# Optimization experiments

Hardware: AMD Instinct MI355X
Metric: run time of the kernel (lower is better)

Reference implementation:

```python
import jax, jax.numpy as jnp
import numpy as np

B = 262144
L, NO, NW = 5, 5, 3          # num_layers, num_ops, num_widths
AD = L * NO * NW             # arch_dim = 75
D, H = 64, 4                 # embed_dim, num_heads
HD = D // H                  # head_dim = 16
EPS = 1e-5


def _ln(x, g, b):
    m = x.mean(-1, keepdims=True)
    v = ((x - m) ** 2).mean(-1, keepdims=True)
    return (x - m) / jnp.sqrt(v + EPS) * g + b


def setup_inputs() -> dict:
    key = jax.random.key(0)
    ks = jax.random.split(key, 16)
    s = 0.05
    return {
        "hw_idx": jax.random.randint(ks[0], (B,), 0, 4),
        "op_indices": jax.random.randint(ks[1], (B, L), 0, NO),
        "width_indices": jax.random.randint(ks[2], (B, L), 0, NW),
        "hw_embed": jax.random.normal(ks[3], (4, D)) * s,
        "W1": jax.random.normal(ks[4], (128, AD)) * s, "b1": jnp.zeros((128,)),
        "W2": jax.random.normal(ks[5], (D, 128)) * s, "b2": jnp.zeros((D,)),
        "ln1_g": jnp.ones((D,)), "ln1_b": jnp.zeros((D,)),
        "in_proj_w": jax.random.normal(ks[6], (3 * D, D)) * s,
        "in_proj_b": jnp.zeros((3 * D,)),
        "out_proj_w": jax.random.normal(ks[7], (D, D)) * s,
        "out_proj_b": jnp.zeros((D,)),
        "ln2_g": jnp.ones((D,)), "ln2_b": jnp.zeros((D,)),
        "W3": jax.random.normal(ks[8], (32, D)) * s, "b3": jnp.zeros((32,)),
        "W4": jax.random.normal(ks[9], (1, 32)) * s, "b4": jnp.zeros((1,)),
    }


def reference(hw_idx, op_indices, width_indices, hw_embed, W1, b1, W2, b2,
              ln1_g, ln1_b, in_proj_w, in_proj_b, out_proj_w, out_proj_b,
              ln2_g, ln2_b, W3, b3, W4, b4):
    # hardware embedding lookup -> [B, D]
    hw_emb = hw_embed[hw_idx]
    # vectorized one-hot arch encoding: [B, L*NO*NW]
    cell = op_indices * NW + width_indices                  # [B, L]
    onehot = jax.nn.one_hot(cell, NO * NW, dtype=jnp.float32).reshape(-1, AD)
    # arch encoder MLP + LayerNorm (dropout = identity at eval)
    h = jax.nn.relu(onehot @ W1.T + b1)
    arch_emb = _ln(h @ W2.T + b2, ln1_g, ln1_b)             # [B, D]
    # combined sequence of 2 tokens: [B, 2, D]
    combined = jnp.stack([hw_emb, arch_emb], axis=1)
    # multi-head self-attention (torch MultiheadAttention, batch_first)
    qkv = combined @ in_proj_w.T + in_proj_b                # [B, 2, 3D]
    q, k, v = jnp.split(qkv, 3, axis=-1)
    q = q.reshape(-1, 2, H, HD); k = k.reshape(-1, 2, H, HD); v = v.reshape(-1, 2, H, HD)
    scores = jnp.einsum('bqhd,bkhd->bhqk', q, k) / np.sqrt(HD)
    attn = jax.nn.softmax(scores, axis=-1)
    ctx = jnp.einsum('bhqk,bkhd->bqhd', attn, v).reshape(-1, 2, D)
    attn_out = ctx @ out_proj_w.T + out_proj_b
    # residual + LayerNorm, mean-pool over the 2 tokens
    x = _ln(attn_out + combined, ln2_g, ln2_b)
    pooled = x.mean(axis=1)                                 # [B, D]
    # prediction head
    latency = jax.nn.relu(pooled @ W3.T + b3) @ W4.T + b4   # [B, 1]
    return latency
```

## Files before the change

### kernel.cpp

```cpp
#include <hip/hip_runtime.h>


using s8v = __attribute__((ext_vector_type(8))) short;
using h8  = __attribute__((ext_vector_type(8))) _Float16;
using f4  = __attribute__((ext_vector_type(4))) float;

#define BTOT 262144

#define WF_W1   0
#define WF_W2   12288
#define WF_IP   20480
#define WF_OP   32768
#define WF_W3   36864
#define WF_HWE  38912

#define OF_ARCH 6400
#define OF_TARG 7552
#define OF_HWI  7680
#define PWS     7696

__device__ __forceinline__ unsigned short f2h(float f) {
  _Float16 h = (_Float16)f;
  return __builtin_bit_cast(unsigned short, h);
}
__device__ __forceinline__ float h2f(unsigned short u) {
  return (float)__builtin_bit_cast(_Float16, u);
}

__device__ __forceinline__ void swz(const float* __restrict__ W,
                                    unsigned short* __restrict__ dst,
                                    int Kreal, int KS, int NT, int t, int stride) {
  const int total = KS * NT * 512;
  for (int i = t; i < total; i += stride) {
    const int j = i & 7, ln = (i >> 3) & 63, fr = i >> 9;
    const int nt = fr % NT, ks = fr / NT;
    const int n = nt * 16 + (ln & 15);
    const int k = ks * 32 + (ln >> 4) * 8 + j;
    dst[i] = (k < Kreal) ? f2h(W[n * Kreal + k]) : (unsigned short)0;
  }
}

__global__ void k_pre(const float* __restrict__ hwe,
                      const float* __restrict__ W1, const float* __restrict__ W2,
                      const float* __restrict__ ipw, const float* __restrict__ opw,
                      const float* __restrict__ W3,
                      unsigned short* __restrict__ ws) {
  const int t = blockIdx.x * 256 + threadIdx.x;
  const int stride = gridDim.x * 256;
  swz(W1,  ws + WF_W1, 75, 3, 8, t, stride);
  swz(W2,  ws + WF_W2, 128, 4, 4, t, stride);
  swz(ipw, ws + WF_IP, 64, 2, 12, t, stride);
  swz(opw, ws + WF_OP, 64, 2, 4, t, stride);
  swz(W3,  ws + WF_W3, 64, 2, 2, t, stride);
  for (int i = t; i < 256; i += stride) ws[WF_HWE + i] = f2h(hwe[i]);
}

__global__ __launch_bounds__(128, 3) void k_fused(
    const int* __restrict__ g_hw,
    const int* __restrict__ g_op, const int* __restrict__ g_wd,
    const float* __restrict__ g_hwe,
    const float* __restrict__ g_b1, const float* __restrict__ g_b2,
    const float* __restrict__ g_ln1g, const float* __restrict__ g_ln1b,
    const float* __restrict__ g_ipb, const float* __restrict__ g_opb,
    const float* __restrict__ g_ln2g, const float* __restrict__ g_ln2b,
    const float* __restrict__ g_b3,  const float* __restrict__ g_W4,
    const float* __restrict__ g_b4,
    const unsigned short* __restrict__ wsf,
    float* __restrict__ g_out) {
  __shared__ __align__(16) unsigned short sm[2 * PWS];
  const int tid = threadIdx.x;
  const int wave = tid >> 6, lane = tid & 63;
  const int quad = lane >> 4, l15 = lane & 15;
  unsigned short* pw = sm + wave * PWS;
  const int m0 = (blockIdx.x * 2 + wave) * 16;

  if (lane < 16) {
    const int smp = m0 + lane;
    pw[OF_HWI + lane] = (unsigned short)g_hw[smp];
#pragma unroll
    for (int l = 0; l < 5; ++l) {
      const int c = 15 * l + g_op[smp * 5 + l] * 3 + g_wd[smp * 5 + l];
      pw[OF_TARG + lane * 8 + l] = (unsigned short)c;
    }
    pw[OF_TARG + lane * 8 + 5] = 0xFFFFu;
    pw[OF_TARG + lane * 8 + 6] = 0xFFFFu;
    pw[OF_TARG + lane * 8 + 7] = 0xFFFFu;
  }
  const s8v trow = *(const s8v*)(pw + OF_TARG + l15 * 8);

  h8 aoh[3];
#pragma unroll
  for (int ks = 0; ks < 3; ++ks) {
    s8v a;
#pragma unroll
    for (int j = 0; j < 8; ++j) {
      const int k = ks * 32 + quad * 8 + j;
      bool hit = false;
#pragma unroll
      for (int l = 0; l < 5; ++l)
        hit = hit || (k == (int)(unsigned short)trow[l]);
      a[j] = hit ? (short)0x3C00 : (short)0;
    }
    aoh[ks] = __builtin_bit_cast(h8, a);
  }

#pragma unroll
  for (int nt = 0; nt < 8; ++nt) {
    f4 acc = {0.f, 0.f, 0.f, 0.f};
#pragma unroll
    for (int ks = 0; ks < 3; ++ks) {
      const h8 bf = *(const h8*)(wsf + WF_W1 + ((ks * 8 + nt) * 64 + lane) * 8);
      acc = __builtin_amdgcn_mfma_f32_16x16x32_f16(aoh[ks], bf, acc, 0, 0, 0);
    }
    const int col = nt * 16 + l15;
    const float bias = g_b1[col];
#pragma unroll
    for (int r = 0; r < 4; ++r) {
      float v = acc[r] + bias;
      v = v > 0.f ? v : 0.f;
      pw[(quad * 4 + r) * 136 + col] = f2h(v);
    }
  }

  h8 a2[4];
#pragma unroll
  for (int ks = 0; ks < 4; ++ks)
    a2[ks] = *(const h8*)(pw + l15 * 136 + ks * 32 + quad * 8);
  f4 acc2[4];
#pragma unroll
  for (int nt = 0; nt < 4; ++nt) {
    f4 acc = {0.f, 0.f, 0.f, 0.f};
#pragma unroll
    for (int ks = 0; ks < 4; ++ks) {
      const h8 bf = *(const h8*)(wsf + WF_W2 + ((ks * 4 + nt) * 64 + lane) * 8);
      acc = __builtin_amdgcn_mfma_f32_16x16x32_f16(a2[ks], bf, acc, 0, 0, 0);
    }
    acc2[nt] = acc;
  }
  {
    float val[4][4];
#pragma unroll
    for (int nt = 0; nt < 4; ++nt) {
      const float bias = g_b2[nt * 16 + l15];
#pragma unroll
      for (int r = 0; r < 4; ++r) val[nt][r] = acc2[nt][r] + bias;
    }
#pragma unroll
    for (int r = 0; r < 4; ++r) {
      float s = val[0][r] + val[1][r] + val[2][r] + val[3][r];
      float q = val[0][r] * val[0][r] + val[1][r] * val[1][r] +
                val[2][r] * val[2][r] + val[3][r] * val[3][r];
#pragma unroll
      for (int off = 1; off <= 8; off <<= 1) {
        s += __shfl_xor(s, off);
        q += __shfl_xor(q, off);
      }
      const float mean = s * (1.f / 64.f);
      const float var  = q * (1.f / 64.f) - mean * mean;
      const float rstd = rsqrtf(var + 1e-5f);
#pragma unroll
      for (int nt = 0; nt < 4; ++nt) {
        const int col = nt * 16 + l15;
        const float gg = g_ln1g[col], bb = g_ln1b[col];
        pw[OF_ARCH + (quad * 4 + r) * 72 + col] =
            f2h((val[nt][r] - mean) * rstd * gg + bb);
      }
    }
  }

  const int hwrow = (int)pw[OF_HWI + l15];
  h8 at0[2], at1[2];
#pragma unroll
  for (int ks = 0; ks < 2; ++ks) {
    at0[ks] = *(const h8*)(wsf + WF_HWE + hwrow * 64 + ks * 32 + quad * 8);
    at1[ks] = *(const h8*)(pw + OF_ARCH + l15 * 72 + ks * 32 + quad * 8);
  }
#pragma unroll
  for (int nt = 0; nt < 12; ++nt) {
    const h8 bf0 = *(const h8*)(wsf + WF_IP + ((0 * 12 + nt) * 64 + lane) * 8);
    const h8 bf1 = *(const h8*)(wsf + WF_IP + ((1 * 12 + nt) * 64 + lane) * 8);
    f4 a0 = {0.f, 0.f, 0.f, 0.f}, a1 = {0.f, 0.f, 0.f, 0.f};
    a0 = __builtin_amdgcn_mfma_f32_16x16x32_f16(at0[0], bf0, a0, 0, 0, 0);
    a0 = __builtin_amdgcn_mfma_f32_16x16x32_f16(at0[1], bf1, a0, 0, 0, 0);
    a1 = __builtin_amdgcn_mfma_f32_16x16x32_f16(at1[0], bf0, a1, 0, 0, 0);
    a1 = __builtin_amdgcn_mfma_f32_16x16x32_f16(at1[1], bf1, a1, 0, 0, 0);
    const int col = nt * 16 + l15;
    const float bias = g_ipb[col];
#pragma unroll
    for (int r = 0; r < 4; ++r) {
      pw[(quad * 4 + r) * 200 + col]      = f2h(a0[r] + bias);
      pw[(16 + quad * 4 + r) * 200 + col] = f2h(a1[r] + bias);
    }
  }

  float ctx[2][16];
  {
    float qv[2][16], kv[2][16], vv[2][16];
#pragma unroll
    for (int tt = 0; tt < 2; ++tt) {
      const unsigned short* base = pw + (tt * 16 + l15) * 200;
#pragma unroll
      for (int c = 0; c < 2; ++c) {
        const h8 qq = *(const h8*)(base + quad * 16 + c * 8);
        const h8 kk = *(const h8*)(base + 64 + quad * 16 + c * 8);
        const h8 vvv = *(const h8*)(base + 128 + quad * 16 + c * 8);
#pragma unroll
        for (int d = 0; d < 8; ++d) {
          qv[tt][c * 8 + d] = (float)qq[d];
          kv[tt][c * 8 + d] = (float)kk[d];
          vv[tt][c * 8 + d] = (float)vvv[d];
        }
      }
    }
    float s00 = 0.f, s01 = 0.f, s10 = 0.f, s11 = 0.f;
#pragma unroll
    for (int d = 0; d < 16; ++d) {
      s00 += qv[0][d] * kv[0][d];
      s01 += qv[0][d] * kv[1][d];
      s10 += qv[1][d] * kv[0][d];
      s11 += qv[1][d] * kv[1][d];
    }
    s00 *= 0.25f; s01 *= 0.25f; s10 *= 0.25f; s11 *= 0.25f;
    const float mA = fmaxf(s00, s01);
    const float e0 = __expf(s00 - mA), e1 = __expf(s01 - mA);
    const float iA = 1.f / (e0 + e1);
    const float a00 = e0 * iA, a01 = e1 * iA;
    const float mB = fmaxf(s10, s11);
    const float f0 = __expf(s10 - mB), f1 = __expf(s11 - mB);
    const float iB = 1.f / (f0 + f1);
    const float a10 = f0 * iB, a11 = f1 * iB;
#pragma unroll
    for (int d = 0; d < 16; ++d) {
      ctx[0][d] = a00 * vv[0][d] + a01 * vv[1][d];
      ctx[1][d] = a10 * vv[0][d] + a11 * vv[1][d];
    }
  }
#pragma unroll
  for (int tt = 0; tt < 2; ++tt)
#pragma unroll
    for (int d = 0; d < 16; d += 2) {
      const unsigned pk = (unsigned)f2h(ctx[tt][d]) |
                          ((unsigned)f2h(ctx[tt][d + 1]) << 16);
      *(unsigned*)(pw + (tt * 16 + l15) * 72 + quad * 16 + d) = pk;
    }

  h8 ca[2][2];
#pragma unroll
  for (int mt = 0; mt < 2; ++mt)
#pragma unroll
    for (int ks = 0; ks < 2; ++ks)
      ca[mt][ks] = *(const h8*)(pw + (mt * 16 + l15) * 72 + ks * 32 + quad * 8);
  f4 oacc[2][4];
#pragma unroll
  for (int nt = 0; nt < 4; ++nt) {
    const h8 bf0 = *(const h8*)(wsf + WF_OP + ((0 * 4 + nt) * 64 + lane) * 8);
    const h8 bf1 = *(const h8*)(wsf + WF_OP + ((1 * 4 + nt) * 64 + lane) * 8);
#pragma unroll
    for (int mt = 0; mt < 2; ++mt) {
      f4 acc = {0.f, 0.f, 0.f, 0.f};
      acc = __builtin_amdgcn_mfma_f32_16x16x32_f16(ca[mt][0], bf0, acc, 0, 0, 0);
      acc = __builtin_amdgcn_mfma_f32_16x16x32_f16(ca[mt][1], bf1, acc, 0, 0, 0);
      oacc[mt][nt] = acc;
    }
  }
  float pool[4][4];
#pragma unroll
  for (int mt = 0; mt < 2; ++mt) {
    float val[4][4];
#pragma unroll
    for (int nt = 0; nt < 4; ++nt) {
      const int col = nt * 16 + l15;
      const float bias = g_opb[col];
#pragma unroll
      for (int r = 0; r < 4; ++r) {
        const int row = quad * 4 + r;
        float res;
        if (mt == 0) {
          const int hr = (int)pw[OF_HWI + row];
          res = g_hwe[hr * 64 + col];
        } else {
          res = h2f(pw[OF_ARCH + row * 72 + col]);
        }
        val[nt][r] = oacc[mt][nt][r] + bias + res;
      }
    }
#pragma unroll
    for (int r = 0; r < 4; ++r) {
      float s = val[0][r] + val[1][r] + val[2][r] + val[3][r];
      float q = val[0][r] * val[0][r] + val[1][r] * val[1][r] +
                val[2][r] * val[2][r] + val[3][r] * val[3][r];
#pragma unroll
      for (int off = 1; off <= 8; off <<= 1) {
        s += __shfl_xor(s, off);
        q += __shfl_xor(q, off);
      }
      const float mean = s * (1.f / 64.f);
      const float var  = q * (1.f / 64.f) - mean * mean;
      const float rstd = rsqrtf(var + 1e-5f);
#pragma unroll
      for (int nt = 0; nt < 4; ++nt) {
        const int col = nt * 16 + l15;
        const float gg = g_ln2g[col], bb = g_ln2b[col];
        const float xn = (val[nt][r] - mean) * rstd * gg + bb;
        if (mt == 0) pool[nt][r] = 0.5f * xn;
        else         pool[nt][r] += 0.5f * xn;
      }
    }
  }
#pragma unroll
  for (int nt = 0; nt < 4; ++nt)
#pragma unroll
    for (int r = 0; r < 4; ++r)
      pw[2304 + (quad * 4 + r) * 72 + nt * 16 + l15] = f2h(pool[nt][r]);

  h8 pa[2];
#pragma unroll
  for (int ks = 0; ks < 2; ++ks)
    pa[ks] = *(const h8*)(pw + 2304 + l15 * 72 + ks * 32 + quad * 8);
  float part[4] = {0.f, 0.f, 0.f, 0.f};
#pragma unroll
  for (int nt = 0; nt < 2; ++nt) {
    const h8 bf0 = *(const h8*)(wsf + WF_W3 + ((0 * 2 + nt) * 64 + lane) * 8);
    const h8 bf1 = *(const h8*)(wsf + WF_W3 + ((1 * 2 + nt) * 64 + lane) * 8);
    f4 acc = {0.f, 0.f, 0.f, 0.f};
    acc = __builtin_amdgcn_mfma_f32_16x16x32_f16(pa[0], bf0, acc, 0, 0, 0);
    acc = __builtin_amdgcn_mfma_f32_16x16x32_f16(pa[1], bf1, acc, 0, 0, 0);
    const int col = nt * 16 + l15;
    const float bias = g_b3[col];
    const float w4v  = g_W4[col];
#pragma unroll
    for (int r = 0; r < 4; ++r) {
      float y = acc[r] + bias;
      y = y > 0.f ? y : 0.f;
      part[r] += y * w4v;
    }
  }
#pragma unroll
  for (int off = 1; off <= 8; off <<= 1)
#pragma unroll
    for (int r = 0; r < 4; ++r)
      part[r] += __shfl_xor(part[r], off);
  const float b4v = g_b4[0];
  if (l15 == 0) {
#pragma unroll
    for (int r = 0; r < 4; ++r)
      g_out[m0 + quad * 4 + r] = part[r] + b4v;
  }
}

extern "C" void kernel_launch(void* const* d_in, const int* in_sizes, int n_in,
                              void* d_out, int out_size, void* d_ws, size_t ws_size,
                              hipStream_t stream) {
  (void)in_sizes; (void)n_in; (void)out_size; (void)ws_size;
  unsigned short* ws = (unsigned short*)d_ws;

  k_pre<<<64, 256, 0, stream>>>(
      (const float*)d_in[3], (const float*)d_in[4], (const float*)d_in[6],
      (const float*)d_in[10], (const float*)d_in[12], (const float*)d_in[16],
      ws);

  k_fused<<<8192, 128, 0, stream>>>(
      (const int*)d_in[0],
      (const int*)d_in[1], (const int*)d_in[2],
      (const float*)d_in[3],
      (const float*)d_in[5], (const float*)d_in[7],
      (const float*)d_in[8], (const float*)d_in[9],
      (const float*)d_in[11], (const float*)d_in[13],
      (const float*)d_in[14], (const float*)d_in[15],
      (const float*)d_in[17], (const float*)d_in[18],
      (const float*)d_in[19],
      ws, (float*)d_out);
}
```

Baseline: 183.5 us.

## Fold b1 into W1, shrink LDS, single-wave blocks, fdot2 attention scores

Folds the first-layer bias b1 into an extra K column of the swizzled W1 weights. The one-hot input now sets a constant-one entry at k=75, so the bias add after the MFMA goes away. The kernel switches to 64-thread single-wave blocks, and the per-block LDS footprint shrinks. To do that, Q/K are stored with a 136 stride and V is kept in registers instead of LDS. Attention scores use packed fp16 fdot2, and softmax weights are exchanged through a small LDS region to compute the context in MFMA layout. The LN1 output is kept in registers for the residual. More registers are live, and fp16 accumulation via fdot2 may change precision slightly.

```diff
diff --git a/kernel.cpp b/kernel.cpp
--- a/kernel.cpp
+++ b/kernel.cpp
@@ -3,6 +3,7 @@
 
 using s8v = __attribute__((ext_vector_type(8))) short;
 using h8  = __attribute__((ext_vector_type(8))) _Float16;
+using h2v = __attribute__((ext_vector_type(2))) _Float16;
 using f4  = __attribute__((ext_vector_type(4))) float;
 
 #define BTOT 262144
@@ -14,10 +15,11 @@
 #define WF_W3   36864
 #define WF_HWE  38912
 
-#define OF_ARCH 6400
-#define OF_TARG 7552
-#define OF_HWI  7680
-#define PWS     7696
+#define OF_WATT 4352
+#define OF_ARCH 4864
+#define OF_TARG 6016
+#define OF_HWI  6144
+#define LDS_TOT 6160
 
 __device__ __forceinline__ unsigned short f2h(float f) {
   _Float16 h = (_Float16)f;
@@ -28,6 +30,7 @@
 }
 
 __device__ __forceinline__ void swz(const float* __restrict__ W,
+                                    const float* __restrict__ bias,
                                     unsigned short* __restrict__ dst,
                                     int Kreal, int KS, int NT, int t, int stride) {
   const int total = KS * NT * 512;
@@ -36,30 +39,34 @@
     const int nt = fr % NT, ks = fr / NT;
     const int n = nt * 16 + (ln & 15);
     const int k = ks * 32 + (ln >> 4) * 8 + j;
-    dst[i] = (k < Kreal) ? f2h(W[n * Kreal + k]) : (unsigned short)0;
+    float v = 0.f;
+    if (k < Kreal) v = W[n * Kreal + k];
+    else if (bias && k == Kreal) v = bias[n];
+    dst[i] = f2h(v);
   }
 }
 
 __global__ void k_pre(const float* __restrict__ hwe,
-                      const float* __restrict__ W1, const float* __restrict__ W2,
+                      const float* __restrict__ W1, const float* __restrict__ b1,
+                      const float* __restrict__ W2,
                       const float* __restrict__ ipw, const float* __restrict__ opw,
                       const float* __restrict__ W3,
                       unsigned short* __restrict__ ws) {
   const int t = blockIdx.x * 256 + threadIdx.x;
   const int stride = gridDim.x * 256;
-  swz(W1,  ws + WF_W1, 75, 3, 8, t, stride);
-  swz(W2,  ws + WF_W2, 128, 4, 4, t, stride);
-  swz(ipw, ws + WF_IP, 64, 2, 12, t, stride);
-  swz(opw, ws + WF_OP, 64, 2, 4, t, stride);
-  swz(W3,  ws + WF_W3, 64, 2, 2, t, stride);
+  swz(W1,  b1,      ws + WF_W1, 75, 3, 8, t, stride);
+  swz(W2,  nullptr, ws + WF_W2, 128, 4, 4, t, stride);
+  swz(ipw, nullptr, ws + WF_IP, 64, 2, 12, t, stride);
+  swz(opw, nullptr, ws + WF_OP, 64, 2, 4, t, stride);
+  swz(W3,  nullptr, ws + WF_W3, 64, 2, 2, t, stride);
   for (int i = t; i < 256; i += stride) ws[WF_HWE + i] = f2h(hwe[i]);
 }
 
-__global__ __launch_bounds__(128, 3) void k_fused(
+__global__ __launch_bounds__(64, 3) void k_fused(
     const int* __restrict__ g_hw,
     const int* __restrict__ g_op, const int* __restrict__ g_wd,
     const float* __restrict__ g_hwe,
-    const float* __restrict__ g_b1, const float* __restrict__ g_b2,
+    const float* __restrict__ g_b2,
     const float* __restrict__ g_ln1g, const float* __restrict__ g_ln1b,
     const float* __restrict__ g_ipb, const float* __restrict__ g_opb,
     const float* __restrict__ g_ln2g, const float* __restrict__ g_ln2b,
@@ -67,12 +74,11 @@
     const float* __restrict__ g_b4,
     const unsigned short* __restrict__ wsf,
     float* __restrict__ g_out) {
-  __shared__ __align__(16) unsigned short sm[2 * PWS];
-  const int tid = threadIdx.x;
-  const int wave = tid >> 6, lane = tid & 63;
+  __shared__ __align__(16) unsigned short sm[LDS_TOT];
+  const int lane = threadIdx.x;
   const int quad = lane >> 4, l15 = lane & 15;
-  unsigned short* pw = sm + wave * PWS;
-  const int m0 = (blockIdx.x * 2 + wave) * 16;
+  unsigned short* pw = sm;
+  const int m0 = blockIdx.x * 16;
 
   if (lane < 16) {
     const int smp = m0 + lane;
@@ -95,7 +101,7 @@
 #pragma unroll
     for (int j = 0; j < 8; ++j) {
       const int k = ks * 32 + quad * 8 + j;
-      bool hit = false;
+      bool hit = (k == 75);
 #pragma unroll
       for (int l = 0; l < 5; ++l)
         hit = hit || (k == (int)(unsigned short)trow[l]);
@@ -113,10 +119,9 @@
       acc = __builtin_amdgcn_mfma_f32_16x16x32_f16(aoh[ks], bf, acc, 0, 0, 0);
     }
     const int col = nt * 16 + l15;
-    const float bias = g_b1[col];
-#pragma unroll
-    for (int r = 0; r < 4; ++r) {
-      float v = acc[r] + bias;
+#pragma unroll
+    for (int r = 0; r < 4; ++r) {
+      float v = acc[r];
       v = v > 0.f ? v : 0.f;
       pw[(quad * 4 + r) * 136 + col] = f2h(v);
     }
@@ -137,6 +142,7 @@
     }
     acc2[nt] = acc;
   }
+  float archres[4][4];
   {
     float val[4][4];
 #pragma unroll
@@ -162,8 +168,9 @@
       for (int nt = 0; nt < 4; ++nt) {
         const int col = nt * 16 + l15;
         const float gg = g_ln1g[col], bb = g_ln1b[col];
-        pw[OF_ARCH + (quad * 4 + r) * 72 + col] =
-            f2h((val[nt][r] - mean) * rstd * gg + bb);
+        const float xn = (val[nt][r] - mean) * rstd * gg + bb;
+        archres[nt][r] = xn;
+        pw[OF_ARCH + (quad * 4 + r) * 72 + col] = f2h(xn);
       }
     }
   }
@@ -175,6 +182,7 @@
     at0[ks] = *(const h8*)(wsf + WF_HWE + hwrow * 64 + ks * 32 + quad * 8);
     at1[ks] = *(const h8*)(pw + OF_ARCH + l15 * 72 + ks * 32 + quad * 8);
   }
+  float vreg[2][4][4];
 #pragma unroll
   for (int nt = 0; nt < 12; ++nt) {
     const h8 bf0 = *(const h8*)(wsf + WF_IP + ((0 * 12 + nt) * 64 + lane) * 8);
@@ -186,62 +194,70 @@
     a1 = __builtin_amdgcn_mfma_f32_16x16x32_f16(at1[1], bf1, a1, 0, 0, 0);
     const int col = nt * 16 + l15;
     const float bias = g_ipb[col];
-#pragma unroll
-    for (int r = 0; r < 4; ++r) {
-      pw[(quad * 4 + r) * 200 + col]      = f2h(a0[r] + bias);
-      pw[(16 + quad * 4 + r) * 200 + col] = f2h(a1[r] + bias);
-    }
-  }
-
-  float ctx[2][16];
+    if (nt < 8) {
+#pragma unroll
+      for (int r = 0; r < 4; ++r) {
+        pw[(quad * 4 + r) * 136 + col]      = f2h(a0[r] + bias);
+        pw[(16 + quad * 4 + r) * 136 + col] = f2h(a1[r] + bias);
+      }
+    } else {
+#pragma unroll
+      for (int r = 0; r < 4; ++r) {
+        vreg[0][nt - 8][r] = a0[r] + bias;
+        vreg[1][nt - 8][r] = a1[r] + bias;
+      }
+    }
+  }
+
   {
-    float qv[2][16], kv[2][16], vv[2][16];
+    h8 qh[2][2], kh[2][2];
 #pragma unroll
     for (int tt = 0; tt < 2; ++tt) {
-      const unsigned short* base = pw + (tt * 16 + l15) * 200;
+      const unsigned short* base = pw + (tt * 16 + l15) * 136;
 #pragma unroll
       for (int c = 0; c < 2; ++c) {
-        const h8 qq = *(const h8*)(base + quad * 16 + c * 8);
-        const h8 kk = *(const h8*)(base + 64 + quad * 16 + c * 8);
-        const h8 vvv = *(const h8*)(base + 128 + quad * 16 + c * 8);
-#pragma unroll
-        for (int d = 0; d < 8; ++d) {
-          qv[tt][c * 8 + d] = (float)qq[d];
-          kv[tt][c * 8 + d] = (float)kk[d];
-          vv[tt][c * 8 + d] = (float)vvv[d];
+        qh[tt][c] = *(const h8*)(base + quad * 16 + c * 8);
+        kh[tt][c] = *(const h8*)(base + 64 + quad * 16 + c * 8);
+      }
+    }
+    float s2[2][2] = {{0.f, 0.f}, {0.f, 0.f}};
+#pragma unroll
+    for (int qt = 0; qt < 2; ++qt)
+#pragma unroll
+      for (int kt = 0; kt < 2; ++kt)
+#pragma unroll
+        for (int c = 0; c < 2; ++c) {
+          const f4 qf = __builtin_bit_cast(f4, qh[qt][c]);
+          const f4 kf = __builtin_bit_cast(f4, kh[kt][c]);
+#pragma unroll
+          for (int u = 0; u < 4; ++u) {
+            const h2v qa = __builtin_bit_cast(h2v, qf[u]);
+            const h2v ka = __builtin_bit_cast(h2v, kf[u]);
+            s2[qt][kt] = __builtin_amdgcn_fdot2(qa, ka, s2[qt][kt], false);
+          }
         }
-      }
-    }
-    float s00 = 0.f, s01 = 0.f, s10 = 0.f, s11 = 0.f;
-#pragma unroll
-    for (int d = 0; d < 16; ++d) {
-      s00 += qv[0][d] * kv[0][d];
-      s01 += qv[0][d] * kv[1][d];
-      s10 += qv[1][d] * kv[0][d];
-      s11 += qv[1][d] * kv[1][d];
-    }
-    s00 *= 0.25f; s01 *= 0.25f; s10 *= 0.25f; s11 *= 0.25f;
+    const float s00 = s2[0][0] * 0.25f, s01 = s2[0][1] * 0.25f;
+    const float s10 = s2[1][0] * 0.25f, s11 = s2[1][1] * 0.25f;
     const float mA = fmaxf(s00, s01);
     const float e0 = __expf(s00 - mA), e1 = __expf(s01 - mA);
     const float iA = 1.f / (e0 + e1);
-    const float a00 = e0 * iA, a01 = e1 * iA;
     const float mB = fmaxf(s10, s11);
     const float f0 = __expf(s10 - mB), f1 = __expf(s11 - mB);
     const float iB = 1.f / (f0 + f1);
-    const float a10 = f0 * iB, a11 = f1 * iB;
-#pragma unroll
-    for (int d = 0; d < 16; ++d) {
-      ctx[0][d] = a00 * vv[0][d] + a01 * vv[1][d];
-      ctx[1][d] = a10 * vv[0][d] + a11 * vv[1][d];
-    }
-  }
-#pragma unroll
-  for (int tt = 0; tt < 2; ++tt)
-#pragma unroll
-    for (int d = 0; d < 16; d += 2) {
-      const unsigned pk = (unsigned)f2h(ctx[tt][d]) |
-                          ((unsigned)f2h(ctx[tt][d + 1]) << 16);
-      *(unsigned*)(pw + (tt * 16 + l15) * 72 + quad * 16 + d) = pk;
+    f4 w = {e0 * iA, e1 * iA, f0 * iB, f1 * iB};
+    ((f4*)(sm + OF_WATT))[l15 * 4 + quad] = w;
+  }
+
+#pragma unroll
+  for (int nt2 = 0; nt2 < 4; ++nt2)
+#pragma unroll
+    for (int r = 0; r < 4; ++r) {
+      const f4 w = ((const f4*)(sm + OF_WATT))[(quad * 4 + r) * 4 + nt2];
+      const float c0 = w[0] * vreg[0][nt2][r] + w[1] * vreg[1][nt2][r];
+      const float c1 = w[2] * vreg[0][nt2][r] + w[3] * vreg[1][nt2][r];
+      const int col = nt2 * 16 + l15;
+      pw[(quad * 4 + r) * 72 + col]      = f2h(c0);
+      pw[(16 + quad * 4 + r) * 72 + col] = f2h(c1);
     }
 
   h8 ca[2][2];
@@ -273,13 +289,12 @@
       const float bias = g_opb[col];
 #pragma unroll
       for (int r = 0; r < 4; ++r) {
-        const int row = quad * 4 + r;
         float res;
         if (mt == 0) {
-          const int hr = (int)pw[OF_HWI + row];
+          const int hr = (int)pw[OF_HWI + quad * 4 + r];
           res = g_hwe[hr * 64 + col];
         } else {
-          res = h2f(pw[OF_ARCH + row * 72 + col]);
+          res = archres[nt][r];
         }
         val[nt][r] = oacc[mt][nt][r] + bias + res;
       }
@@ -355,15 +370,15 @@
   unsigned short* ws = (unsigned short*)d_ws;
 
   k_pre<<<64, 256, 0, stream>>>(
-      (const float*)d_in[3], (const float*)d_in[4], (const float*)d_in[6],
-      (const float*)d_in[10], (const float*)d_in[12], (const float*)d_in[16],
-      ws);
-
-  k_fused<<<8192, 128, 0, stream>>>(
+      (const float*)d_in[3], (const float*)d_in[4], (const float*)d_in[5],
+      (const float*)d_in[6], (const float*)d_in[10], (const float*)d_in[12],
+      (const float*)d_in[16], ws);
+
+  k_fused<<<16384, 64, 0, stream>>>(
       (const int*)d_in[0],
       (const int*)d_in[1], (const int*)d_in[2],
       (const float*)d_in[3],
-      (const float*)d_in[5], (const float*)d_in[7],
+      (const float*)d_in[7],
       (const float*)d_in[8], (const float*)d_in[9],
       (const float*)d_in[11], (const float*)d_in[13],
       (const float*)d_in[14], (const float*)d_in[15],
```

Measured after the change: 205.5 us. 1.12x slower.
